# Performance work log

Hardware: AMD Instinct MI355X
Metric: run time of the kernel (lower is better)

The kernel has to match this reference:

```python
import jax, jax.numpy as jnp
import numpy as np

N_VOCAB = 50000   # pretrained_emb.size(0) == n_input; also number of graph nodes
N_FEAT = 128      # pretrained_emb.size(1)
N_OUT = 64        # n_output
N_EDGES = 1600000
BN_EPS = 1e-5


def _bn(x, gamma, beta):
    # BatchNorm1d in training mode: batch stats over the node dimension
    mean = jnp.mean(x, axis=0)
    var = jnp.var(x, axis=0)
    return gamma * (x - mean) * jax.lax.rsqrt(var + BN_EPS) + beta


def _gcn_layer(x, W, b, row, col, vals, n_nodes):
    # SpGraphConvLayer: support = x @ W ; out = spmm(adj, support) + b
    support = x @ W                              # [N, out]
    msgs = vals[:, None] * support[col]          # [E, out] gather
    out = jax.ops.segment_sum(msgs, row, num_segments=n_nodes)  # scatter-add
    return out + b


def setup_inputs() -> dict:
    key = jax.random.key(0)
    ks = jax.random.split(key, 12)
    vertices = jnp.arange(N_VOCAB, dtype=jnp.int32)
    row = jax.random.randint(ks[0], (N_EDGES,), 0, N_VOCAB, dtype=jnp.int32)
    col = jax.random.randint(ks[1], (N_EDGES,), 0, N_VOCAB, dtype=jnp.int32)
    adj_vals = jax.random.uniform(ks[2], (N_EDGES,), dtype=jnp.float32)
    emb = jax.random.normal(ks[3], (N_VOCAB, N_FEAT), dtype=jnp.float32)
    W1 = jax.random.normal(ks[4], (N_FEAT, N_FEAT), dtype=jnp.float32) / np.sqrt(N_FEAT)
    b1 = jnp.zeros((N_FEAT,), jnp.float32)
    gamma1 = jnp.ones((N_FEAT,), jnp.float32)
    beta1 = jnp.zeros((N_FEAT,), jnp.float32)
    W2 = jax.random.normal(ks[5], (N_FEAT, N_OUT), dtype=jnp.float32) / np.sqrt(N_FEAT)
    b2 = jnp.zeros((N_OUT,), jnp.float32)
    gamma2 = jnp.ones((N_OUT,), jnp.float32)
    beta2 = jnp.zeros((N_OUT,), jnp.float32)
    Wm = jax.random.normal(ks[6], (N_VOCAB, N_OUT), dtype=jnp.float32) / np.sqrt(N_VOCAB)
    bm = jnp.zeros((N_OUT,), jnp.float32)
    return {"emb": emb, "W1": W1, "b1": b1, "gamma1": gamma1, "beta1": beta1,
            "W2": W2, "b2": b2, "gamma2": gamma2, "beta2": beta2,
            "Wm": Wm, "bm": bm,
            "vertices": vertices, "row": row, "col": col, "adj_vals": adj_vals}


def reference(emb, W1, b1, gamma1, beta1, W2, b2, gamma2, beta2, Wm, bm,
              vertices, row, col, adj_vals):
    n = vertices.shape[0]
    x = emb[vertices]                                       # frozen embedding lookup [N, F]
    x = jax.nn.relu(_bn(_gcn_layer(x, W1, b1, row, col, adj_vals, n), gamma1, beta1))
    # dropout is identity in eval / deterministic reference
    x = jax.nn.relu(_bn(_gcn_layer(x, W2, b2, row, col, adj_vals, n), gamma2, beta2))
    # MaskLinear: gather mask weight rows at vertices, elementwise mul, sum over nodes
    x = jnp.sum(x * Wm[vertices], axis=0) + bm              # [n_output]
    return jax.nn.sigmoid(x)
```

## Files before the change

kernel.cpp:

```cpp
#include <hip/hip_runtime.h>
#include <hip/hip_bf16.h>
#include <math.h>

#define N_NODES 50000
#define NEDGE 1600000
#define BN_EPS 1e-5f
#define G1_BLOCKS 1563
#define EB 1563
#define SB 128
#define NBUCK 196
#define BCAP 10240

__device__ inline float bf2f(ushort u) {
  union { unsigned i; float f; } v;
  v.i = ((unsigned)u) << 16;
  return v.f;
}
__device__ inline ushort f2bf(float x) {
  __hip_bfloat16 b = __float2bfloat16(x);
  return *(ushort*)&b;
}

__global__ __launch_bounds__(256) void gemm1_bin_kernel(
    const float4* __restrict__ X4, const float4* __restrict__ W4,
    ushort* __restrict__ C, const int4* __restrict__ row4,
    const int4* __restrict__ col4, const float4* __restrict__ vals4,
    int* __restrict__ gcur, uint2* __restrict__ bdata) {
  __shared__ float4 sW[64 * 32];
  __shared__ float4 sX[32 * 32];
  const int t = threadIdx.x;

  if (blockIdx.x & 1) {
    int* bcnt = (int*)sW;
    int* bbase = bcnt + 256;
    int* lcur = bbase + 256;
    uint2* stage = (uint2*)(lcur + 256);
    for (int i = t; i < NBUCK; i += 256) bcnt[i] = 0;
    __syncthreads();
    int i4 = (blockIdx.x >> 1) * 256 + t;
    bool valid = i4 < NEDGE / 4;
    if (valid) {
      int4 r = row4[i4];
      int4 c = col4[i4];
      float4 v = vals4[i4];
      atomicAdd(&bcnt[r.x >> 8], 1);
      atomicAdd(&bcnt[r.y >> 8], 1);
      atomicAdd(&bcnt[r.z >> 8], 1);
      atomicAdd(&bcnt[r.w >> 8], 1);
      stage[t * 4 + 0] = make_uint2((unsigned)r.x,
                                    ((unsigned)c.x << 16) | f2bf(v.x));
      stage[t * 4 + 1] = make_uint2((unsigned)r.y,
                                    ((unsigned)c.y << 16) | f2bf(v.y));
      stage[t * 4 + 2] = make_uint2((unsigned)r.z,
                                    ((unsigned)c.z << 16) | f2bf(v.z));
      stage[t * 4 + 3] = make_uint2((unsigned)r.w,
                                    ((unsigned)c.w << 16) | f2bf(v.w));
    }
    __syncthreads();
    if (t < NBUCK) {
      lcur[t] = 0;
      bbase[t] = bcnt[t] ? atomicAdd(&gcur[t], bcnt[t]) : 0;
    }
    __syncthreads();
    if (valid) {
#pragma unroll
      for (int k = 0; k < 4; ++k) {
        uint2 e = stage[t * 4 + k];
        int b = e.x >> 8;
        int pos = bbase[b] + atomicAdd(&lcur[b], 1);
        if (pos < BCAP) bdata[(long)b * BCAP + pos] = e;
      }
    }
    return;
  }

  float* Xl = (float*)sX;
  const int r0 = (blockIdx.x >> 1) * 32;

  for (int i = t; i < 1024; i += 256) {
    int rr = i >> 5;
    int r = r0 + rr;
    sX[i] = (r < N_NODES) ? X4[(long)r * 32 + (i & 31)]
                          : make_float4(0.f, 0.f, 0.f, 0.f);
  }

  const int tx = t & 31;
  const int ty = t >> 5;
  float acc[4][4] = {{0.f}};

  for (int kt = 0; kt < 2; ++kt) {
    __syncthreads();
    for (int i = t; i < 2048; i += 256) sW[i] = W4[kt * 2048 + i];
    __syncthreads();
    const int kbase = kt * 64;
#pragma unroll 8
    for (int kk = 0; kk < 64; ++kk) {
      float4 wv = sW[kk * 32 + tx];
      float x0 = Xl[(ty * 4 + 0) * 128 + kbase + kk];
      float x1 = Xl[(ty * 4 + 1) * 128 + kbase + kk];
      float x2 = Xl[(ty * 4 + 2) * 128 + kbase + kk];
      float x3 = Xl[(ty * 4 + 3) * 128 + kbase + kk];
      acc[0][0] += x0 * wv.x; acc[0][1] += x0 * wv.y;
      acc[0][2] += x0 * wv.z; acc[0][3] += x0 * wv.w;
      acc[1][0] += x1 * wv.x; acc[1][1] += x1 * wv.y;
      acc[1][2] += x1 * wv.z; acc[1][3] += x1 * wv.w;
      acc[2][0] += x2 * wv.x; acc[2][1] += x2 * wv.y;
      acc[2][2] += x2 * wv.z; acc[2][3] += x2 * wv.w;
      acc[3][0] += x3 * wv.x; acc[3][1] += x3 * wv.y;
      acc[3][2] += x3 * wv.z; acc[3][3] += x3 * wv.w;
    }
  }
  for (int j = 0; j < 4; ++j) {
    int r = r0 + ty * 4 + j;
    if (r < N_NODES) {
      ushort4 o;
      o.x = f2bf(acc[j][0]); o.y = f2bf(acc[j][1]);
      o.z = f2bf(acc[j][2]); o.w = f2bf(acc[j][3]);
      *(ushort4*)&C[(long)r * 128 + tx * 4] = o;
    }
  }
}

__global__ __launch_bounds__(256) void bscan_kernel(
    const int* __restrict__ gcur, int* __restrict__ boffg) {
  int t = threadIdx.x;
  int v = (t < NBUCK) ? gcur[t] : 0;
  __shared__ int sc[256];
  sc[t] = v;
  __syncthreads();
  for (int off = 1; off < 256; off <<= 1) {
    int x = (t >= off) ? sc[t - off] : 0;
    __syncthreads();
    sc[t] += x;
    __syncthreads();
  }
  if (t < NBUCK) boffg[t] = sc[t] - v;
}

__global__ __launch_bounds__(512) void sort_kernel(
    const uint2* __restrict__ bdata, const int* __restrict__ gcur,
    const int* __restrict__ boffg, int* __restrict__ rowptr,
    unsigned* __restrict__ ep) {
  const int b = blockIdx.x;
  const int t = threadIdx.x;
  __shared__ int rcnt[256], roff[256], cur[256];
  __shared__ unsigned eps[BCAP];
  int total = gcur[b];
  if (total > BCAP) total = BCAP;
  int base = boffg[b];
  if (t < 256) rcnt[t] = 0;
  __syncthreads();
  for (int i = t; i < total; i += 512) {
    uint2 e = bdata[(long)b * BCAP + i];
    atomicAdd(&rcnt[e.x & 255], 1);
  }
  __syncthreads();
  if (t < 256) roff[t] = rcnt[t];
  __syncthreads();
  for (int off = 1; off < 256; off <<= 1) {
    int x = 0;
    if (t < 256 && t >= off) x = roff[t - off];
    __syncthreads();
    if (t < 256) roff[t] += x;
    __syncthreads();
  }
  if (t < 256) {
    int excl = roff[t] - rcnt[t];
    cur[t] = excl;
    int grow = b * 256 + t;
    if (grow < N_NODES) rowptr[grow] = base + excl;
  }
  if (b == NBUCK - 1 && t == 0) rowptr[N_NODES] = NEDGE;
  __syncthreads();
  for (int i = t; i < total; i += 512) {
    uint2 e = bdata[(long)b * BCAP + i];
    int p = atomicAdd(&cur[e.x & 255], 1);
    eps[p] = e.y;
  }
  __syncthreads();
  for (int i = t; i < total; i += 512) ep[base + i] = eps[i];
}

__global__ __launch_bounds__(256) void gather128_kernel(
    const int* __restrict__ rowptr, const unsigned* __restrict__ ep,
    const ushort* __restrict__ S, ushort2* __restrict__ H) {
  int r = (blockIdx.x * 256 + threadIdx.x) >> 6;
  int lane = threadIdx.x & 63;
  if (r >= N_NODES) return;
  int b = rowptr[r], e2 = rowptr[r + 1];
  float a0x = 0.f, a0y = 0.f, a1x = 0.f, a1y = 0.f;
  float a2x = 0.f, a2y = 0.f, a3x = 0.f, a3y = 0.f;
  int e = b;
  for (; e + 3 < e2; e += 4) {
    unsigned u0 = ep[e], u1 = ep[e + 1], u2 = ep[e + 2], u3 = ep[e + 3];
    ushort2 s0 = ((const ushort2*)(S + (long)(u0 >> 16) * 128))[lane];
    ushort2 s1 = ((const ushort2*)(S + (long)(u1 >> 16) * 128))[lane];
    ushort2 s2 = ((const ushort2*)(S + (long)(u2 >> 16) * 128))[lane];
    ushort2 s3 = ((const ushort2*)(S + (long)(u3 >> 16) * 128))[lane];
    float v0 = bf2f((ushort)u0), v1 = bf2f((ushort)u1);
    float v2 = bf2f((ushort)u2), v3 = bf2f((ushort)u3);
    a0x += v0 * bf2f(s0.x); a0y += v0 * bf2f(s0.y);
    a1x += v1 * bf2f(s1.x); a1y += v1 * bf2f(s1.y);
    a2x += v2 * bf2f(s2.x); a2y += v2 * bf2f(s2.y);
    a3x += v3 * bf2f(s3.x); a3y += v3 * bf2f(s3.y);
  }
  for (; e < e2; ++e) {
    unsigned u0 = ep[e];
    float v0 = bf2f((ushort)u0);
    ushort2 s0 = ((const ushort2*)(S + (long)(u0 >> 16) * 128))[lane];
    a0x += v0 * bf2f(s0.x); a0y += v0 * bf2f(s0.y);
  }
  float hx = (a0x + a1x) + (a2x + a3x);
  float hy = (a0y + a1y) + (a2y + a3y);
  H[(long)r * 64 + lane] = make_ushort2(f2bf(hx), f2bf(hy));
}

__global__ __launch_bounds__(256) void statsbf_part_kernel(
    const ushort* __restrict__ H, float* __restrict__ part_s,
    float* __restrict__ part_q) {
  const int t = threadIdx.x;
  const int cg = t & 31;
  const int rg = t >> 5;
  float sum0 = 0.f, sum1 = 0.f, sum2 = 0.f, sum3 = 0.f;
  float sq0 = 0.f, sq1 = 0.f, sq2 = 0.f, sq3 = 0.f;
  for (int r = blockIdx.x * 8 + rg; r < N_NODES; r += SB * 8) {
    ushort4 u = *(const ushort4*)(H + (long)r * 128 + cg * 4);
    float x0 = bf2f(u.x), x1 = bf2f(u.y), x2 = bf2f(u.z), x3 = bf2f(u.w);
    sum0 += x0; sq0 += x0 * x0;
    sum1 += x1; sq1 += x1 * x1;
    sum2 += x2; sq2 += x2 * x2;
    sum3 += x3; sq3 += x3 * x3;
  }
  __shared__ float lds[8][128];
  lds[rg][cg * 4 + 0] = sum0; lds[rg][cg * 4 + 1] = sum1;
  lds[rg][cg * 4 + 2] = sum2; lds[rg][cg * 4 + 3] = sum3;
  __syncthreads();
  if (t < 128) {
    float x = 0.f;
#pragma unroll
    for (int g = 0; g < 8; ++g) x += lds[g][t];
    part_s[blockIdx.x * 128 + t] = x;
  }
  __syncthreads();
  lds[rg][cg * 4 + 0] = sq0; lds[rg][cg * 4 + 1] = sq1;
  lds[rg][cg * 4 + 2] = sq2; lds[rg][cg * 4 + 3] = sq3;
  __syncthreads();
  if (t < 128) {
    float x = 0.f;
#pragma unroll
    for (int g = 0; g < 8; ++g) x += lds[g][t];
    part_q[blockIdx.x * 128 + t] = x;
  }
}

template <int NC>
__global__ void stats_reduce_kernel(const float* __restrict__ part_s,
                                    const float* __restrict__ part_q,
                                    float* __restrict__ s,
                                    float* __restrict__ ss) {
  int t = threadIdx.x;
  float a = 0.f, b = 0.f;
  for (int i = 0; i < SB; ++i) {
    a += part_s[i * NC + t];
    b += part_q[i * NC + t];
  }
  s[t] = a;
  ss[t] = b;
}

__global__ __launch_bounds__(256) void gemm2_kernel(
    const ushort* __restrict__ Hbf, const float4* __restrict__ W4,
    const float* __restrict__ s1, const float* __restrict__ ss1,
    const float* __restrict__ gamma, const float* __restrict__ beta,
    ushort* __restrict__ C) {
  __shared__ float4 sW[128 * 16];
  __shared__ float4 sX[32 * 32];
  __shared__ float sA[128], sB[128];
  const int t = threadIdx.x;

  if (t < 128) {
    float mean = s1[t] * (1.0f / N_NODES);
    float var = ss1[t] * (1.0f / N_NODES) - mean * mean;
    float a = gamma[t] * rsqrtf(var + BN_EPS);
    sA[t] = a;
    sB[t] = beta[t] - a * mean;
  }
  for (int i = t; i < 2048; i += 256) sW[i] = W4[i];
  __syncthreads();

  const int r0 = blockIdx.x * 32;
  for (int i = t; i < 1024; i += 256) {
    int rr = i >> 5;
    int r = r0 + rr;
    int c4 = i & 31;
    float4 v = make_float4(0.f, 0.f, 0.f, 0.f);
    if (r < N_NODES) {
      ushort4 u = *(const ushort4*)(Hbf + (long)r * 128 + c4 * 4);
      float4 a4 = *(const float4*)&sA[c4 * 4];
      float4 b4 = *(const float4*)&sB[c4 * 4];
      v.x = fmaxf(a4.x * bf2f(u.x) + b4.x, 0.f);
      v.y = fmaxf(a4.y * bf2f(u.y) + b4.y, 0.f);
      v.z = fmaxf(a4.z * bf2f(u.z) + b4.z, 0.f);
      v.w = fmaxf(a4.w * bf2f(u.w) + b4.w, 0.f);
    }
    sX[i] = v;
  }
  __syncthreads();

  const int tx = t & 15;
  const int ty = t >> 4;
  float acc[2][4] = {{0.f}};
  float* Xl = (float*)sX;
#pragma unroll 8
  for (int k = 0; k < 128; ++k) {
    float4 wv = sW[k * 16 + tx];
    float x0 = Xl[(ty * 2 + 0) * 128 + k];
    float x1 = Xl[(ty * 2 + 1) * 128 + k];
    acc[0][0] += x0 * wv.x; acc[0][1] += x0 * wv.y;
    acc[0][2] += x0 * wv.z; acc[0][3] += x0 * wv.w;
    acc[1][0] += x1 * wv.x; acc[1][1] += x1 * wv.y;
    acc[1][2] += x1 * wv.z; acc[1][3] += x1 * wv.w;
  }
  for (int j = 0; j < 2; ++j) {
    int r = r0 + ty * 2 + j;
    if (r < N_NODES) {
      ushort4 o;
      o.x = f2bf(acc[j][0]); o.y = f2bf(acc[j][1]);
      o.z = f2bf(acc[j][2]); o.w = f2bf(acc[j][3]);
      *(ushort4*)&C[(long)r * 64 + tx * 4] = o;
    }
  }
}

__global__ __launch_bounds__(256) void gather64_kernel(
    const int* __restrict__ rowptr, const unsigned* __restrict__ ep,
    const ushort* __restrict__ S, float2* __restrict__ H) {
  int r = (blockIdx.x * 256 + threadIdx.x) >> 5;
  int sub = threadIdx.x & 31;
  if (r >= N_NODES) return;
  int b = rowptr[r], e2 = rowptr[r + 1];
  float a0x = 0.f, a0y = 0.f, a1x = 0.f, a1y = 0.f;
  float a2x = 0.f, a2y = 0.f, a3x = 0.f, a3y = 0.f;
  int e = b;
  for (; e + 3 < e2; e += 4) {
    unsigned u0 = ep[e], u1 = ep[e + 1], u2 = ep[e + 2], u3 = ep[e + 3];
    ushort2 s0 = ((const ushort2*)(S + (long)(u0 >> 16) * 64))[sub];
    ushort2 s1 = ((const ushort2*)(S + (long)(u1 >> 16) * 64))[sub];
    ushort2 s2 = ((const ushort2*)(S + (long)(u2 >> 16) * 64))[sub];
    ushort2 s3 = ((const ushort2*)(S + (long)(u3 >> 16) * 64))[sub];
    float v0 = bf2f((ushort)u0), v1 = bf2f((ushort)u1);
    float v2 = bf2f((ushort)u2), v3 = bf2f((ushort)u3);
    a0x += v0 * bf2f(s0.x); a0y += v0 * bf2f(s0.y);
    a1x += v1 * bf2f(s1.x); a1y += v1 * bf2f(s1.y);
    a2x += v2 * bf2f(s2.x); a2y += v2 * bf2f(s2.y);
    a3x += v3 * bf2f(s3.x); a3y += v3 * bf2f(s3.y);
  }
  for (; e < e2; ++e) {
    unsigned u0 = ep[e];
    float v0 = bf2f((ushort)u0);
    ushort2 s0 = ((const ushort2*)(S + (long)(u0 >> 16) * 64))[sub];
    a0x += v0 * bf2f(s0.x); a0y += v0 * bf2f(s0.y);
  }
  H[(long)r * 32 + sub] = make_float2((a0x + a1x) + (a2x + a3x),
                                      (a0y + a1y) + (a2y + a3y));
}

__global__ __launch_bounds__(256) void stats64_part_kernel(
    const float* __restrict__ H, float* __restrict__ part_s,
    float* __restrict__ part_q) {
  const int t = threadIdx.x;
  const int c = t & 63;
  const int rg = t >> 6;
  float sum = 0.f, sq = 0.f;
  for (int r = blockIdx.x * 4 + rg; r < N_NODES; r += SB * 4) {
    float x = H[(long)r * 64 + c];
    sum += x;
    sq += x * x;
  }
  __shared__ float lds[4][64];
  lds[rg][c] = sum;
  __syncthreads();
  if (t < 64)
    part_s[blockIdx.x * 64 + t] =
        lds[0][t] + lds[1][t] + lds[2][t] + lds[3][t];
  __syncthreads();
  lds[rg][c] = sq;
  __syncthreads();
  if (t < 64)
    part_q[blockIdx.x * 64 + t] =
        lds[0][t] + lds[1][t] + lds[2][t] + lds[3][t];
}

__global__ __launch_bounds__(256) void final_part_kernel(
    const float* __restrict__ H, const float* __restrict__ Wm,
    const float* __restrict__ s2, const float* __restrict__ ss2,
    const float* __restrict__ gamma, const float* __restrict__ beta,
    float* __restrict__ partF) {
  const int t = threadIdx.x;
  const int c = t & 63;
  const int rg = t >> 6;
  float mean = s2[c] * (1.0f / N_NODES);
  float var = ss2[c] * (1.0f / N_NODES) - mean * mean;
  float a = gamma[c] * rsqrtf(var + BN_EPS);
  float b = beta[c] - a * mean;
  float sum = 0.f;
  for (int r = blockIdx.x * 4 + rg; r < N_NODES; r += SB * 4) {
    float x = fmaxf(a * H[(long)r * 64 + c] + b, 0.f);
    sum += x * Wm[(long)r * 64 + c];
  }
  __shared__ float lds[4][64];
  lds[rg][c] = sum;
  __syncthreads();
  if (t < 64)
    partF[blockIdx.x * 64 + t] =
        lds[0][t] + lds[1][t] + lds[2][t] + lds[3][t];
}

__global__ void writeout_kernel(const float* __restrict__ partF,
                                const float* __restrict__ bm,
                                float* __restrict__ out) {
  int t = threadIdx.x;
  float x = bm[t];
  for (int i = 0; i < SB; ++i) x += partF[i * 64 + t];
  out[t] = 1.0f / (1.0f + expf(-x));
}

extern "C" void kernel_launch(void* const* d_in, const int* in_sizes, int n_in,
                              void* d_out, int out_size, void* d_ws,
                              size_t ws_size, hipStream_t stream) {
  const float* emb  = (const float*)d_in[0];
  const float* W1   = (const float*)d_in[1];
  const float* g1   = (const float*)d_in[3];
  const float* be1  = (const float*)d_in[4];
  const float* W2   = (const float*)d_in[5];
  const float* g2   = (const float*)d_in[7];
  const float* be2  = (const float*)d_in[8];
  const float* Wm   = (const float*)d_in[9];
  const float* bm   = (const float*)d_in[10];
  const int* row    = (const int*)d_in[12];
  const int* col    = (const int*)d_in[13];
  const float* vals = (const float*)d_in[14];

  ushort*   sup    = (ushort*)d_ws;
  ushort*   h1     = sup + 6400000;
  float*    h2     = (float*)(h1 + 6400000);
  uint2*    bdata  = (uint2*)h1;
  unsigned* ep     = (unsigned*)(h2 + 3200000);
  int*      rowptr = (int*)(ep + 1600000);
  int*      gcur   = rowptr + 50001;
  int*      boffg  = gcur + 256;
  float*    part_s = (float*)(boffg + 256);
  float*    part_q = part_s + SB * 128;
  float*    partF  = part_q + SB * 128;
  float*    s1     = partF + SB * 64;
  float*    ss1    = s1 + 128;
  float*    s2     = ss1 + 128;
  float*    ss2    = s2 + 64;
  float*    out = (float*)d_out;

  hipMemsetAsync(gcur, 0, 256 * sizeof(int), stream);

  gemm1_bin_kernel<<<G1_BLOCKS + EB, 256, 0, stream>>>(
      (const float4*)emb, (const float4*)W1, sup, (const int4*)row,
      (const int4*)col, (const float4*)vals, gcur, bdata);

  bscan_kernel<<<1, 256, 0, stream>>>(gcur, boffg);
  sort_kernel<<<NBUCK, 512, 0, stream>>>(bdata, gcur, boffg, rowptr, ep);

  gather128_kernel<<<(N_NODES * 64 + 255) / 256, 256, 0, stream>>>(
      rowptr, ep, sup, (ushort2*)h1);
  statsbf_part_kernel<<<SB, 256, 0, stream>>>(h1, part_s, part_q);
  stats_reduce_kernel<128><<<1, 128, 0, stream>>>(part_s, part_q, s1, ss1);

  gemm2_kernel<<<G1_BLOCKS, 256, 0, stream>>>(h1, (const float4*)W2, s1, ss1,
                                              g1, be1, sup);
  gather64_kernel<<<(N_NODES * 32 + 255) / 256, 256, 0, stream>>>(
      rowptr, ep, sup, (float2*)h2);
  stats64_part_kernel<<<SB, 256, 0, stream>>>(h2, part_s, part_q);
  stats_reduce_kernel<64><<<1, 64, 0, stream>>>(part_s, part_q, s2, ss2);

  final_part_kernel<<<SB, 256, 0, stream>>>(h2, Wm, s2, ss2, g2, be2, partF);
  writeout_kernel<<<1, 64, 0, stream>>>(partF, bm, out);
}
```

Measured before the change: 267.7 us.

## Fold tiny reduction kernels into producers via last-block tickets; unroll gathers by 8

Removes four single-block launches (bucket scan, two stats reductions, writeout). The bucket prefix scan is recomputed redundantly inside every sort block, and each final reduction runs in the last-arriving block, chosen by an atomic ticket counter after a threadfence. The ticket counters are zeroed together with the bucket counters by one enlarged memset. Separately, both SpMM gather kernels now keep 8 independent edge loads in flight with 8 accumulator pairs instead of 4, for more memory-level parallelism at the cost of more registers.

```diff
diff --git a/kernel.cpp b/kernel.cpp
--- a/kernel.cpp
+++ b/kernel.cpp
@@ -121,33 +121,27 @@
   }
 }
 
-__global__ __launch_bounds__(256) void bscan_kernel(
-    const int* __restrict__ gcur, int* __restrict__ boffg) {
-  int t = threadIdx.x;
-  int v = (t < NBUCK) ? gcur[t] : 0;
-  __shared__ int sc[256];
-  sc[t] = v;
-  __syncthreads();
-  for (int off = 1; off < 256; off <<= 1) {
-    int x = (t >= off) ? sc[t - off] : 0;
-    __syncthreads();
-    sc[t] += x;
-    __syncthreads();
-  }
-  if (t < NBUCK) boffg[t] = sc[t] - v;
-}
-
 __global__ __launch_bounds__(512) void sort_kernel(
     const uint2* __restrict__ bdata, const int* __restrict__ gcur,
-    const int* __restrict__ boffg, int* __restrict__ rowptr,
-    unsigned* __restrict__ ep) {
+    int* __restrict__ rowptr, unsigned* __restrict__ ep) {
   const int b = blockIdx.x;
   const int t = threadIdx.x;
   __shared__ int rcnt[256], roff[256], cur[256];
+  __shared__ int gsc[256];
   __shared__ unsigned eps[BCAP];
+  int gv = (t < NBUCK) ? gcur[t] : 0;
+  if (t < 256) gsc[t] = gv;
+  __syncthreads();
+  for (int off = 1; off < 256; off <<= 1) {
+    int x = 0;
+    if (t < 256 && t >= off) x = gsc[t - off];
+    __syncthreads();
+    if (t < 256) gsc[t] += x;
+    __syncthreads();
+  }
   int total = gcur[b];
   if (total > BCAP) total = BCAP;
-  int base = boffg[b];
+  int base = gsc[b] - gcur[b];
   if (t < 256) rcnt[t] = 0;
   __syncthreads();
   for (int i = t; i < total; i += 512) {
@@ -188,36 +182,43 @@
   int lane = threadIdx.x & 63;
   if (r >= N_NODES) return;
   int b = rowptr[r], e2 = rowptr[r + 1];
-  float a0x = 0.f, a0y = 0.f, a1x = 0.f, a1y = 0.f;
-  float a2x = 0.f, a2y = 0.f, a3x = 0.f, a3y = 0.f;
+  float ax[8], ay[8];
+#pragma unroll
+  for (int i = 0; i < 8; ++i) { ax[i] = 0.f; ay[i] = 0.f; }
   int e = b;
-  for (; e + 3 < e2; e += 4) {
-    unsigned u0 = ep[e], u1 = ep[e + 1], u2 = ep[e + 2], u3 = ep[e + 3];
-    ushort2 s0 = ((const ushort2*)(S + (long)(u0 >> 16) * 128))[lane];
-    ushort2 s1 = ((const ushort2*)(S + (long)(u1 >> 16) * 128))[lane];
-    ushort2 s2 = ((const ushort2*)(S + (long)(u2 >> 16) * 128))[lane];
-    ushort2 s3 = ((const ushort2*)(S + (long)(u3 >> 16) * 128))[lane];
-    float v0 = bf2f((ushort)u0), v1 = bf2f((ushort)u1);
-    float v2 = bf2f((ushort)u2), v3 = bf2f((ushort)u3);
-    a0x += v0 * bf2f(s0.x); a0y += v0 * bf2f(s0.y);
-    a1x += v1 * bf2f(s1.x); a1y += v1 * bf2f(s1.y);
-    a2x += v2 * bf2f(s2.x); a2y += v2 * bf2f(s2.y);
-    a3x += v3 * bf2f(s3.x); a3y += v3 * bf2f(s3.y);
+  for (; e + 7 < e2; e += 8) {
+    unsigned u[8];
+    ushort2 s[8];
+#pragma unroll
+    for (int i = 0; i < 8; ++i) u[i] = ep[e + i];
+#pragma unroll
+    for (int i = 0; i < 8; ++i)
+      s[i] = ((const ushort2*)(S + (long)(u[i] >> 16) * 128))[lane];
+#pragma unroll
+    for (int i = 0; i < 8; ++i) {
+      float v = bf2f((ushort)u[i]);
+      ax[i] += v * bf2f(s[i].x);
+      ay[i] += v * bf2f(s[i].y);
+    }
   }
   for (; e < e2; ++e) {
     unsigned u0 = ep[e];
     float v0 = bf2f((ushort)u0);
     ushort2 s0 = ((const ushort2*)(S + (long)(u0 >> 16) * 128))[lane];
-    a0x += v0 * bf2f(s0.x); a0y += v0 * bf2f(s0.y);
-  }
-  float hx = (a0x + a1x) + (a2x + a3x);
-  float hy = (a0y + a1y) + (a2y + a3y);
+    ax[0] += v0 * bf2f(s0.x);
+    ay[0] += v0 * bf2f(s0.y);
+  }
+  float hx = ((ax[0] + ax[1]) + (ax[2] + ax[3])) +
+             ((ax[4] + ax[5]) + (ax[6] + ax[7]));
+  float hy = ((ay[0] + ay[1]) + (ay[2] + ay[3])) +
+             ((ay[4] + ay[5]) + (ay[6] + ay[7]));
   H[(long)r * 64 + lane] = make_ushort2(f2bf(hx), f2bf(hy));
 }
 
-__global__ __launch_bounds__(256) void statsbf_part_kernel(
+__global__ __launch_bounds__(256) void statsbf_kernel(
     const ushort* __restrict__ H, float* __restrict__ part_s,
-    float* __restrict__ part_q) {
+    float* __restrict__ part_q, int* __restrict__ ticket,
+    float* __restrict__ s, float* __restrict__ ss) {
   const int t = threadIdx.x;
   const int cg = t & 31;
   const int rg = t >> 5;
@@ -251,21 +252,19 @@
     for (int g = 0; g < 8; ++g) x += lds[g][t];
     part_q[blockIdx.x * 128 + t] = x;
   }
-}
-
-template <int NC>
-__global__ void stats_reduce_kernel(const float* __restrict__ part_s,
-                                    const float* __restrict__ part_q,
-                                    float* __restrict__ s,
-                                    float* __restrict__ ss) {
-  int t = threadIdx.x;
-  float a = 0.f, b = 0.f;
-  for (int i = 0; i < SB; ++i) {
-    a += part_s[i * NC + t];
-    b += part_q[i * NC + t];
-  }
-  s[t] = a;
-  ss[t] = b;
+  __shared__ bool isLast;
+  __threadfence();
+  if (t == 0) isLast = (atomicAdd(ticket, 1) == SB - 1);
+  __syncthreads();
+  if (isLast && t < 128) {
+    float a = 0.f, bq = 0.f;
+    for (int i = 0; i < SB; ++i) {
+      a += part_s[i * 128 + t];
+      bq += part_q[i * 128 + t];
+    }
+    s[t] = a;
+    ss[t] = bq;
+  }
 }
 
 __global__ __launch_bounds__(256) void gemm2_kernel(
@@ -339,35 +338,43 @@
   int sub = threadIdx.x & 31;
   if (r >= N_NODES) return;
   int b = rowptr[r], e2 = rowptr[r + 1];
-  float a0x = 0.f, a0y = 0.f, a1x = 0.f, a1y = 0.f;
-  float a2x = 0.f, a2y = 0.f, a3x = 0.f, a3y = 0.f;
+  float ax[8], ay[8];
+#pragma unroll
+  for (int i = 0; i < 8; ++i) { ax[i] = 0.f; ay[i] = 0.f; }
   int e = b;
-  for (; e + 3 < e2; e += 4) {
-    unsigned u0 = ep[e], u1 = ep[e + 1], u2 = ep[e + 2], u3 = ep[e + 3];
-    ushort2 s0 = ((const ushort2*)(S + (long)(u0 >> 16) * 64))[sub];
-    ushort2 s1 = ((const ushort2*)(S + (long)(u1 >> 16) * 64))[sub];
-    ushort2 s2 = ((const ushort2*)(S + (long)(u2 >> 16) * 64))[sub];
-    ushort2 s3 = ((const ushort2*)(S + (long)(u3 >> 16) * 64))[sub];
-    float v0 = bf2f((ushort)u0), v1 = bf2f((ushort)u1);
-    float v2 = bf2f((ushort)u2), v3 = bf2f((ushort)u3);
-    a0x += v0 * bf2f(s0.x); a0y += v0 * bf2f(s0.y);
-    a1x += v1 * bf2f(s1.x); a1y += v1 * bf2f(s1.y);
-    a2x += v2 * bf2f(s2.x); a2y += v2 * bf2f(s2.y);
-    a3x += v3 * bf2f(s3.x); a3y += v3 * bf2f(s3.y);
+  for (; e + 7 < e2; e += 8) {
+    unsigned u[8];
+    ushort2 s[8];
+#pragma unroll
+    for (int i = 0; i < 8; ++i) u[i] = ep[e + i];
+#pragma unroll
+    for (int i = 0; i < 8; ++i)
+      s[i] = ((const ushort2*)(S + (long)(u[i] >> 16) * 64))[sub];
+#pragma unroll
+    for (int i = 0; i < 8; ++i) {
+      float v = bf2f((ushort)u[i]);
+      ax[i] += v * bf2f(s[i].x);
+      ay[i] += v * bf2f(s[i].y);
+    }
   }
   for (; e < e2; ++e) {
     unsigned u0 = ep[e];
     float v0 = bf2f((ushort)u0);
     ushort2 s0 = ((const ushort2*)(S + (long)(u0 >> 16) * 64))[sub];
-    a0x += v0 * bf2f(s0.x); a0y += v0 * bf2f(s0.y);
-  }
-  H[(long)r * 32 + sub] = make_float2((a0x + a1x) + (a2x + a3x),
-                                      (a0y + a1y) + (a2y + a3y));
-}
-
-__global__ __launch_bounds__(256) void stats64_part_kernel(
+    ax[0] += v0 * bf2f(s0.x);
+    ay[0] += v0 * bf2f(s0.y);
+  }
+  float hx = ((ax[0] + ax[1]) + (ax[2] + ax[3])) +
+             ((ax[4] + ax[5]) + (ax[6] + ax[7]));
+  float hy = ((ay[0] + ay[1]) + (ay[2] + ay[3])) +
+             ((ay[4] + ay[5]) + (ay[6] + ay[7]));
+  H[(long)r * 32 + sub] = make_float2(hx, hy);
+}
+
+__global__ __launch_bounds__(256) void stats64_kernel(
     const float* __restrict__ H, float* __restrict__ part_s,
-    float* __restrict__ part_q) {
+    float* __restrict__ part_q, int* __restrict__ ticket,
+    float* __restrict__ s, float* __restrict__ ss) {
   const int t = threadIdx.x;
   const int c = t & 63;
   const int rg = t >> 6;
@@ -389,13 +396,27 @@
   if (t < 64)
     part_q[blockIdx.x * 64 + t] =
         lds[0][t] + lds[1][t] + lds[2][t] + lds[3][t];
-}
-
-__global__ __launch_bounds__(256) void final_part_kernel(
+  __shared__ bool isLast;
+  __threadfence();
+  if (t == 0) isLast = (atomicAdd(ticket, 1) == SB - 1);
+  __syncthreads();
+  if (isLast && t < 64) {
+    float a = 0.f, bq = 0.f;
+    for (int i = 0; i < SB; ++i) {
+      a += part_s[i * 64 + t];
+      bq += part_q[i * 64 + t];
+    }
+    s[t] = a;
+    ss[t] = bq;
+  }
+}
+
+__global__ __launch_bounds__(256) void final_kernel(
     const float* __restrict__ H, const float* __restrict__ Wm,
     const float* __restrict__ s2, const float* __restrict__ ss2,
     const float* __restrict__ gamma, const float* __restrict__ beta,
-    float* __restrict__ partF) {
+    const float* __restrict__ bm, float* __restrict__ partF,
+    int* __restrict__ ticket, float* __restrict__ out) {
   const int t = threadIdx.x;
   const int c = t & 63;
   const int rg = t >> 6;
@@ -414,15 +435,15 @@
   if (t < 64)
     partF[blockIdx.x * 64 + t] =
         lds[0][t] + lds[1][t] + lds[2][t] + lds[3][t];
-}
-
-__global__ void writeout_kernel(const float* __restrict__ partF,
-                                const float* __restrict__ bm,
-                                float* __restrict__ out) {
-  int t = threadIdx.x;
-  float x = bm[t];
-  for (int i = 0; i < SB; ++i) x += partF[i * 64 + t];
-  out[t] = 1.0f / (1.0f + expf(-x));
+  __shared__ bool isLast;
+  __threadfence();
+  if (t == 0) isLast = (atomicAdd(ticket, 1) == SB - 1);
+  __syncthreads();
+  if (isLast && t < 64) {
+    float x = bm[t];
+    for (int i = 0; i < SB; ++i) x += partF[i * 64 + t];
+    out[t] = 1.0f / (1.0f + expf(-x));
+  }
 }
 
 extern "C" void kernel_launch(void* const* d_in, const int* in_sizes, int n_in,
@@ -448,8 +469,8 @@
   unsigned* ep     = (unsigned*)(h2 + 3200000);
   int*      rowptr = (int*)(ep + 1600000);
   int*      gcur   = rowptr + 50001;
-  int*      boffg  = gcur + 256;
-  float*    part_s = (float*)(boffg + 256);
+  int*      tick   = gcur + 256;
+  float*    part_s = (float*)(tick + 8);
   float*    part_q = part_s + SB * 128;
   float*    partF  = part_q + SB * 128;
   float*    s1     = partF + SB * 64;
@@ -458,27 +479,26 @@
   float*    ss2    = s2 + 64;
   float*    out = (float*)d_out;
 
-  hipMemsetAsync(gcur, 0, 256 * sizeof(int), stream);
+  hipMemsetAsync(gcur, 0, 264 * sizeof(int), stream);
 
   gemm1_bin_kernel<<<G1_BLOCKS + EB, 256, 0, stream>>>(
       (const float4*)emb, (const float4*)W1, sup, (const int4*)row,
       (const int4*)col, (const float4*)vals, gcur, bdata);
 
-  bscan_kernel<<<1, 256, 0, stream>>>(gcur, boffg);
-  sort_kernel<<<NBUCK, 512, 0, stream>>>(bdata, gcur, boffg, rowptr, ep);
+  sort_kernel<<<NBUCK, 512, 0, stream>>>(bdata, gcur, rowptr, ep);
 
   gather128_kernel<<<(N_NODES * 64 + 255) / 256, 256, 0, stream>>>(
       rowptr, ep, sup, (ushort2*)h1);
-  statsbf_part_kernel<<<SB, 256, 0, stream>>>(h1, part_s, part_q);
-  stats_reduce_kernel<128><<<1, 128, 0, stream>>>(part_s, part_q, s1, ss1);
+  statsbf_kernel<<<SB, 256, 0, stream>>>(h1, part_s, part_q, &tick[0], s1,
+                                         ss1);
 
   gemm2_kernel<<<G1_BLOCKS, 256, 0, stream>>>(h1, (const float4*)W2, s1, ss1,
                                               g1, be1, sup);
   gather64_kernel<<<(N_NODES * 32 + 255) / 256, 256, 0, stream>>>(
       rowptr, ep, sup, (float2*)h2);
-  stats64_part_kernel<<<SB, 256, 0, stream>>>(h2, part_s, part_q);
-  stats_reduce_kernel<64><<<1, 64, 0, stream>>>(part_s, part_q, s2, ss2);
-
-  final_part_kernel<<<SB, 256, 0, stream>>>(h2, Wm, s2, ss2, g2, be2, partF);
-  writeout_kernel<<<1, 64, 0, stream>>>(partF, bm, out);
-}
+  stats64_kernel<<<SB, 256, 0, stream>>>(h2, part_s, part_q, &tick[1], s2,
+                                         ss2);
+
+  final_kernel<<<SB, 256, 0, stream>>>(h2, Wm, s2, ss2, g2, be2, bm, partF,
+                                       &tick[2], out);
+}
```

Result: slower. 277.1 us (+3.5%).

## Use bf16 MFMA for both dense GEMMs with prepacked weight fragments

Applied to the files above, without the earlier changes.

Both dense projections switch from scalar FP32 FMA loops to bf16 MFMA 16x16x32 instructions. A new small kernel converts W1 and W2 to bf16 and packs them into per-lane fragment layout. Activation tiles are staged in LDS as bf16 with a padded row stride, and B fragments are read straight from global memory. This cuts ALU time and LDS footprint, at the cost of rounding the inputs and weights to bf16 and one extra kernel launch.

```diff
diff --git a/kernel.cpp b/kernel.cpp
--- a/kernel.cpp
+++ b/kernel.cpp
@@ -11,6 +11,9 @@
 #define NBUCK 196
 #define BCAP 10240
 
+typedef __attribute__((ext_vector_type(8))) short bf16x8;
+typedef __attribute__((ext_vector_type(4))) float f32x4;
+
 __device__ inline float bf2f(ushort u) {
   union { unsigned i; float f; } v;
   v.i = ((unsigned)u) << 16;
@@ -21,17 +24,42 @@
   return *(ushort*)&b;
 }
 
+__global__ __launch_bounds__(256) void wpack_kernel(
+    const float* __restrict__ W1, const float* __restrict__ W2,
+    ushort* __restrict__ Wp1, ushort* __restrict__ Wp2) {
+  int task = blockIdx.x * 256 + threadIdx.x;
+  if (task < 2048) {
+    int tt = task >> 6, l = task & 63;
+    int kc = tt >> 3, cn = tt & 7;
+    int k0 = kc * 32 + (l >> 4) * 8, c = cn * 16 + (l & 15);
+    ushort tmp[8];
+#pragma unroll
+    for (int i = 0; i < 8; ++i) tmp[i] = f2bf(W1[(long)(k0 + i) * 128 + c]);
+#pragma unroll
+    for (int i = 0; i < 8; ++i) Wp1[task * 8 + i] = tmp[i];
+  } else if (task < 3072) {
+    int t2 = task - 2048;
+    int tt = t2 >> 6, l = t2 & 63;
+    int kc = tt >> 2, cn = tt & 3;
+    int k0 = kc * 32 + (l >> 4) * 8, c = cn * 16 + (l & 15);
+    ushort tmp[8];
+#pragma unroll
+    for (int i = 0; i < 8; ++i) tmp[i] = f2bf(W2[(long)(k0 + i) * 64 + c]);
+#pragma unroll
+    for (int i = 0; i < 8; ++i) Wp2[t2 * 8 + i] = tmp[i];
+  }
+}
+
 __global__ __launch_bounds__(256) void gemm1_bin_kernel(
-    const float4* __restrict__ X4, const float4* __restrict__ W4,
+    const float4* __restrict__ X4, const ushort* __restrict__ Wp1,
     ushort* __restrict__ C, const int4* __restrict__ row4,
     const int4* __restrict__ col4, const float4* __restrict__ vals4,
     int* __restrict__ gcur, uint2* __restrict__ bdata) {
-  __shared__ float4 sW[64 * 32];
-  __shared__ float4 sX[32 * 32];
+  __shared__ uint4 smem[768];
   const int t = threadIdx.x;
 
   if (blockIdx.x & 1) {
-    int* bcnt = (int*)sW;
+    int* bcnt = (int*)smem;
     int* bbase = bcnt + 256;
     int* lcur = bbase + 256;
     uint2* stage = (uint2*)(lcur + 256);
@@ -74,49 +102,51 @@
     return;
   }
 
-  float* Xl = (float*)sX;
+  ushort* sXb = (ushort*)smem;
   const int r0 = (blockIdx.x >> 1) * 32;
 
   for (int i = t; i < 1024; i += 256) {
-    int rr = i >> 5;
+    int rr = i >> 5, c4 = i & 31;
     int r = r0 + rr;
-    sX[i] = (r < N_NODES) ? X4[(long)r * 32 + (i & 31)]
-                          : make_float4(0.f, 0.f, 0.f, 0.f);
-  }
-
-  const int tx = t & 31;
-  const int ty = t >> 5;
-  float acc[4][4] = {{0.f}};
-
-  for (int kt = 0; kt < 2; ++kt) {
-    __syncthreads();
-    for (int i = t; i < 2048; i += 256) sW[i] = W4[kt * 2048 + i];
-    __syncthreads();
-    const int kbase = kt * 64;
-#pragma unroll 8
-    for (int kk = 0; kk < 64; ++kk) {
-      float4 wv = sW[kk * 32 + tx];
-      float x0 = Xl[(ty * 4 + 0) * 128 + kbase + kk];
-      float x1 = Xl[(ty * 4 + 1) * 128 + kbase + kk];
-      float x2 = Xl[(ty * 4 + 2) * 128 + kbase + kk];
-      float x3 = Xl[(ty * 4 + 3) * 128 + kbase + kk];
-      acc[0][0] += x0 * wv.x; acc[0][1] += x0 * wv.y;
-      acc[0][2] += x0 * wv.z; acc[0][3] += x0 * wv.w;
-      acc[1][0] += x1 * wv.x; acc[1][1] += x1 * wv.y;
-      acc[1][2] += x1 * wv.z; acc[1][3] += x1 * wv.w;
-      acc[2][0] += x2 * wv.x; acc[2][1] += x2 * wv.y;
-      acc[2][2] += x2 * wv.z; acc[2][3] += x2 * wv.w;
-      acc[3][0] += x3 * wv.x; acc[3][1] += x3 * wv.y;
-      acc[3][2] += x3 * wv.z; acc[3][3] += x3 * wv.w;
-    }
-  }
-  for (int j = 0; j < 4; ++j) {
-    int r = r0 + ty * 4 + j;
-    if (r < N_NODES) {
-      ushort4 o;
-      o.x = f2bf(acc[j][0]); o.y = f2bf(acc[j][1]);
-      o.z = f2bf(acc[j][2]); o.w = f2bf(acc[j][3]);
-      *(ushort4*)&C[(long)r * 128 + tx * 4] = o;
+    float4 v = (r < N_NODES) ? X4[(long)r * 32 + c4]
+                             : make_float4(0.f, 0.f, 0.f, 0.f);
+    ushort4 u;
+    u.x = f2bf(v.x); u.y = f2bf(v.y); u.z = f2bf(v.z); u.w = f2bf(v.w);
+    *(ushort4*)&sXb[rr * 136 + c4 * 4] = u;
+  }
+  __syncthreads();
+
+  const int w = t >> 6, l = t & 63;
+  const int rm = w >> 1;
+  const int cn0 = (w & 1) * 4;
+  const int arow = rm * 16 + (l & 15);
+  const int kg = l >> 4;
+
+  bf16x8 a[4];
+#pragma unroll
+  for (int kc = 0; kc < 4; ++kc)
+    a[kc] = *(const bf16x8*)&sXb[arow * 136 + kc * 32 + kg * 8];
+
+  f32x4 acc[4];
+#pragma unroll
+  for (int cn = 0; cn < 4; ++cn) acc[cn] = (f32x4){0.f, 0.f, 0.f, 0.f};
+
+#pragma unroll
+  for (int cn = 0; cn < 4; ++cn) {
+#pragma unroll
+    for (int kc = 0; kc < 4; ++kc) {
+      bf16x8 b = *(const bf16x8*)&Wp1[((kc * 8 + cn0 + cn) * 64 + l) * 8];
+      acc[cn] = __builtin_amdgcn_mfma_f32_16x16x32_bf16(a[kc], b, acc[cn],
+                                                        0, 0, 0);
+    }
+  }
+#pragma unroll
+  for (int cn = 0; cn < 4; ++cn) {
+#pragma unroll
+    for (int j = 0; j < 4; ++j) {
+      int r = r0 + rm * 16 + kg * 4 + j;
+      if (r < N_NODES)
+        C[(long)r * 128 + (cn0 + cn) * 16 + (l & 15)] = f2bf(acc[cn][j]);
     }
   }
 }
@@ -269,12 +299,11 @@
 }
 
 __global__ __launch_bounds__(256) void gemm2_kernel(
-    const ushort* __restrict__ Hbf, const float4* __restrict__ W4,
+    const ushort* __restrict__ Hbf, const ushort* __restrict__ Wp2,
     const float* __restrict__ s1, const float* __restrict__ ss1,
     const float* __restrict__ gamma, const float* __restrict__ beta,
     ushort* __restrict__ C) {
-  __shared__ float4 sW[128 * 16];
-  __shared__ float4 sX[32 * 32];
+  __shared__ ushort sXb[32 * 136];
   __shared__ float sA[128], sB[128];
   const int t = threadIdx.x;
 
@@ -285,49 +314,56 @@
     sA[t] = a;
     sB[t] = beta[t] - a * mean;
   }
-  for (int i = t; i < 2048; i += 256) sW[i] = W4[i];
   __syncthreads();
 
   const int r0 = blockIdx.x * 32;
   for (int i = t; i < 1024; i += 256) {
-    int rr = i >> 5;
+    int rr = i >> 5, c4 = i & 31;
     int r = r0 + rr;
-    int c4 = i & 31;
-    float4 v = make_float4(0.f, 0.f, 0.f, 0.f);
+    ushort4 o = make_ushort4(0, 0, 0, 0);
     if (r < N_NODES) {
       ushort4 u = *(const ushort4*)(Hbf + (long)r * 128 + c4 * 4);
-      float4 a4 = *(const float4*)&sA[c4 * 4];
-      float4 b4 = *(const float4*)&sB[c4 * 4];
-      v.x = fmaxf(a4.x * bf2f(u.x) + b4.x, 0.f);
-      v.y = fmaxf(a4.y * bf2f(u.y) + b4.y, 0.f);
-      v.z = fmaxf(a4.z * bf2f(u.z) + b4.z, 0.f);
-      v.w = fmaxf(a4.w * bf2f(u.w) + b4.w, 0.f);
-    }
-    sX[i] = v;
-  }
-  __syncthreads();
-
-  const int tx = t & 15;
-  const int ty = t >> 4;
-  float acc[2][4] = {{0.f}};
-  float* Xl = (float*)sX;
-#pragma unroll 8
-  for (int k = 0; k < 128; ++k) {
-    float4 wv = sW[k * 16 + tx];
-    float x0 = Xl[(ty * 2 + 0) * 128 + k];
-    float x1 = Xl[(ty * 2 + 1) * 128 + k];
-    acc[0][0] += x0 * wv.x; acc[0][1] += x0 * wv.y;
-    acc[0][2] += x0 * wv.z; acc[0][3] += x0 * wv.w;
-    acc[1][0] += x1 * wv.x; acc[1][1] += x1 * wv.y;
-    acc[1][2] += x1 * wv.z; acc[1][3] += x1 * wv.w;
-  }
-  for (int j = 0; j < 2; ++j) {
-    int r = r0 + ty * 2 + j;
-    if (r < N_NODES) {
-      ushort4 o;
-      o.x = f2bf(acc[j][0]); o.y = f2bf(acc[j][1]);
-      o.z = f2bf(acc[j][2]); o.w = f2bf(acc[j][3]);
-      *(ushort4*)&C[(long)r * 64 + tx * 4] = o;
+      float x0 = fmaxf(sA[c4 * 4 + 0] * bf2f(u.x) + sB[c4 * 4 + 0], 0.f);
+      float x1 = fmaxf(sA[c4 * 4 + 1] * bf2f(u.y) + sB[c4 * 4 + 1], 0.f);
+      float x2 = fmaxf(sA[c4 * 4 + 2] * bf2f(u.z) + sB[c4 * 4 + 2], 0.f);
+      float x3 = fmaxf(sA[c4 * 4 + 3] * bf2f(u.w) + sB[c4 * 4 + 3], 0.f);
+      o = make_ushort4(f2bf(x0), f2bf(x1), f2bf(x2), f2bf(x3));
+    }
+    *(ushort4*)&sXb[rr * 136 + c4 * 4] = o;
+  }
+  __syncthreads();
+
+  const int w = t >> 6, l = t & 63;
+  const int rm = w >> 1;
+  const int cn0 = (w & 1) * 2;
+  const int arow = rm * 16 + (l & 15);
+  const int kg = l >> 4;
+
+  bf16x8 a[4];
+#pragma unroll
+  for (int kc = 0; kc < 4; ++kc)
+    a[kc] = *(const bf16x8*)&sXb[arow * 136 + kc * 32 + kg * 8];
+
+  f32x4 acc[2];
+#pragma unroll
+  for (int cn = 0; cn < 2; ++cn) acc[cn] = (f32x4){0.f, 0.f, 0.f, 0.f};
+
+#pragma unroll
+  for (int cn = 0; cn < 2; ++cn) {
+#pragma unroll
+    for (int kc = 0; kc < 4; ++kc) {
+      bf16x8 b = *(const bf16x8*)&Wp2[((kc * 4 + cn0 + cn) * 64 + l) * 8];
+      acc[cn] = __builtin_amdgcn_mfma_f32_16x16x32_bf16(a[kc], b, acc[cn],
+                                                        0, 0, 0);
+    }
+  }
+#pragma unroll
+  for (int cn = 0; cn < 2; ++cn) {
+#pragma unroll
+    for (int j = 0; j < 4; ++j) {
+      int r = r0 + rm * 16 + kg * 4 + j;
+      if (r < N_NODES)
+        C[(long)r * 64 + (cn0 + cn) * 16 + (l & 15)] = f2bf(acc[cn][j]);
     }
   }
 }
@@ -449,7 +485,9 @@
   int*      rowptr = (int*)(ep + 1600000);
   int*      gcur   = rowptr + 50001;
   int*      boffg  = gcur + 256;
-  float*    part_s = (float*)(boffg + 256);
+  ushort*   Wp1    = (ushort*)(boffg + 256);
+  ushort*   Wp2    = Wp1 + 16384;
+  float*    part_s = (float*)(Wp2 + 8192);
   float*    part_q = part_s + SB * 128;
   float*    partF  = part_q + SB * 128;
   float*    s1     = partF + SB * 64;
@@ -460,9 +498,11 @@
 
   hipMemsetAsync(gcur, 0, 256 * sizeof(int), stream);
 
+  wpack_kernel<<<12, 256, 0, stream>>>(W1, W2, Wp1, Wp2);
+
   gemm1_bin_kernel<<<G1_BLOCKS + EB, 256, 0, stream>>>(
-      (const float4*)emb, (const float4*)W1, sup, (const int4*)row,
-      (const int4*)col, (const float4*)vals, gcur, bdata);
+      (const float4*)emb, Wp1, sup, (const int4*)row, (const int4*)col,
+      (const float4*)vals, gcur, bdata);
 
   bscan_kernel<<<1, 256, 0, stream>>>(gcur, boffg);
   sort_kernel<<<NBUCK, 512, 0, stream>>>(bdata, gcur, boffg, rowptr, ep);
@@ -472,8 +512,7 @@
   statsbf_part_kernel<<<SB, 256, 0, stream>>>(h1, part_s, part_q);
   stats_reduce_kernel<128><<<1, 128, 0, stream>>>(part_s, part_q, s1, ss1);
 
-  gemm2_kernel<<<G1_BLOCKS, 256, 0, stream>>>(h1, (const float4*)W2, s1, ss1,
-                                              g1, be1, sup);
+  gemm2_kernel<<<G1_BLOCKS, 256, 0, stream>>>(h1, Wp2, s1, ss1, g1, be1, sup);
   gather64_kernel<<<(N_NODES * 32 + 255) / 256, 256, 0, stream>>>(
       rowptr, ep, sup, (float2*)h2);
   stats64_part_kernel<<<SB, 256, 0, stream>>>(h2, part_s, part_q);
```

New measurement: 256.9 us. 1.04x faster.
